# Optimization experiments

Hardware: AMD Instinct MI355X
Metric: run time of the kernel (lower is better)

Reference implementation:

```python
import math
import jax, jax.numpy as jnp
import numpy as np

B, T, C, H = 2, 2048, 1024, 16
HD = C // H  # head dim = 64


def setup_inputs() -> dict:
    key = jax.random.key(0)
    k1, k2, k3 = jax.random.split(key, 3)
    x = jax.random.normal(k1, (B, T, C), dtype=jnp.float32)
    w_attn = jax.random.normal(k2, (C, 3 * C), dtype=jnp.float32) * (1.0 / math.sqrt(C))
    b_attn = jnp.zeros((3 * C,), dtype=jnp.float32)
    w_proj = jax.random.normal(k3, (C, C), dtype=jnp.float32) * (1.0 / math.sqrt(C))
    b_proj = jnp.zeros((C,), dtype=jnp.float32)
    return {"x": x, "w_attn": w_attn, "b_attn": b_attn, "w_proj": w_proj, "b_proj": b_proj}


def reference(x, w_attn, b_attn, w_proj, b_proj):
    b, t, c = x.shape
    hd = c // H
    # fused QKV projection: [B,T,3C]
    qkv = x @ w_attn + b_attn
    q, k, v = jnp.split(qkv, 3, axis=2)
    # [B,T,C] -> [B,H,T,hd]
    q = q.reshape(b, t, H, hd).transpose(0, 2, 1, 3)
    k = k.reshape(b, t, H, hd).transpose(0, 2, 1, 3)
    v = v.reshape(b, t, H, hd).transpose(0, 2, 1, 3)
    # scaled scores: [B,H,T,T]
    att = jnp.einsum("bhqd,bhkd->bhqk", q, k) * (1.0 / math.sqrt(hd))
    # causal mask: keep lower triangle, -inf elsewhere
    causal = jnp.tril(jnp.ones((t, t), dtype=bool))
    att = jnp.where(causal[None, None, :, :], att, jnp.float32(-jnp.inf))
    att = jax.nn.softmax(att, axis=-1)
    # attention-weighted values: [B,H,T,hd] -> [B,T,C]
    y = jnp.einsum("bhqk,bhkd->bhqd", att, v)
    y = y.transpose(0, 2, 1, 3).reshape(b, t, c)
    # output projection (dropout prob 0 => identity)
    return y @ w_proj + b_proj
```

## Files before the change

### kernel.cpp

```cpp
#include <hip/hip_runtime.h>
#include <type_traits>


typedef __bf16 bf16x8 __attribute__((ext_vector_type(8)));
typedef __bf16 bf16x4 __attribute__((ext_vector_type(4)));
typedef short shortx4 __attribute__((ext_vector_type(4)));
typedef float f32x4 __attribute__((ext_vector_type(4)));

#define B_ 2
#define T_ 2048
#define C_ 1024
#define H_ 16
#define HD_ 64
#define ROWS_ (B_ * T_)
#define N3C_ (3 * C_)

__device__ inline void gll16(const void* g, void* l) {
    __builtin_amdgcn_global_load_lds(
        (const __attribute__((address_space(1))) void*)g,
        (__attribute__((address_space(3))) void*)l, 16, 0, 0);
}

__device__ inline f32x4 mfma16x16x16(bf16x4 a, bf16x4 b, f32x4 c) {
#if defined(__HIP_DEVICE_COMPILE__)
#if __has_builtin(__builtin_amdgcn_mfma_f32_16x16x16bf16_1k)
    return __builtin_amdgcn_mfma_f32_16x16x16bf16_1k(
        __builtin_bit_cast(shortx4, a), __builtin_bit_cast(shortx4, b), c, 0, 0, 0);
#else
    return __builtin_amdgcn_mfma_f32_16x16x16_bf16(
        __builtin_bit_cast(shortx4, a), __builtin_bit_cast(shortx4, b), c, 0, 0, 0);
#endif
#else
    (void)a; (void)b;
    return c;
#endif
}

__device__ inline float v_exp2(float x) {
#if defined(__HIP_DEVICE_COMPILE__)
    float r;
    asm("v_exp_f32 %0, %1" : "=v"(r) : "v"(x));
    return r;
#else
    return x;
#endif
}

__device__ inline float bias_at(const void* bias, int col, bool in_bf) {
    return in_bf ? (float)((const __bf16*)bias)[col] : ((const float*)bias)[col];
}

__global__ void detect_dtype(const unsigned* __restrict__ w, unsigned* __restrict__ flag) {
    int lane = threadIdx.x & 63;
    int cnt = 0;
#pragma unroll
    for (int i = 0; i < 4; ++i) {
        unsigned v = w[lane * 4 + i];
        unsigned e = (v >> 7) & 0xFFu;
        cnt += (e >= 116u && e <= 134u) ? 1 : 0;
    }
#pragma unroll
    for (int off = 1; off < 64; off <<= 1) cnt += __shfl_xor(cnt, off, 64);
    if (lane == 0) *flag = (cnt >= 128) ? 1u : 0u;
}

__global__ __launch_bounds__(256) void convert_to_bf16(const void* __restrict__ src,
                                                       __bf16* __restrict__ dst, int n,
                                                       const unsigned* __restrict__ flag) {
    bool isbf = (*flag != 0u);
    int i = (blockIdx.x * 256 + threadIdx.x) * 8;
    if (i >= n) return;
    if (isbf) {
        *(bf16x8*)&dst[i] = *(const bf16x8*)((const __bf16*)src + i);
    } else {
        const float4* s4 = (const float4*)src;
        float4 a = s4[i / 4], b = s4[i / 4 + 1];
        bf16x8 v;
        v[0] = (__bf16)a.x; v[1] = (__bf16)a.y; v[2] = (__bf16)a.z; v[3] = (__bf16)a.w;
        v[4] = (__bf16)b.x; v[5] = (__bf16)b.y; v[6] = (__bf16)b.z; v[7] = (__bf16)b.w;
        *(bf16x8*)&dst[i] = v;
    }
}

__global__ __launch_bounds__(256) void transpose2(const void* __restrict__ wa,
                                                  __bf16* __restrict__ wat,
                                                  const void* __restrict__ wp,
                                                  __bf16* __restrict__ wpt,
                                                  const unsigned* __restrict__ flag) {
    int z = blockIdx.z;
    if (z && blockIdx.x >= 16) return;
    const void* src = z ? wp : wa;
    __bf16* dst = z ? wpt : wat;
    int R = C_, Cc = z ? C_ : N3C_;

    __shared__ __align__(16) __bf16 tile[64][65];
    bool isbf = (*flag != 0u);
    const __bf16* sb = (const __bf16*)src;
    const float* sf = (const float*)src;
    int cb = blockIdx.x * 64, rb = blockIdx.y * 64;
    for (int i = threadIdx.x; i < 4096; i += 256) {
        int r = i >> 6, c = i & 63;
        size_t idx = (size_t)(rb + r) * Cc + cb + c;
        tile[r][c] = isbf ? sb[idx] : (__bf16)sf[idx];
    }
    __syncthreads();
    for (int i = threadIdx.x; i < 4096; i += 256) {
        int r = i >> 6, c = i & 63;
        dst[(size_t)(cb + r) * R + rb + c] = tile[c][r];
    }
}

__global__ __launch_bounds__(256) void gemm_qkv(const __bf16* __restrict__ A,
                                                const __bf16* __restrict__ Bt,
                                                const void* __restrict__ bias,
                                                __bf16* __restrict__ qg,
                                                __bf16* __restrict__ kg,
                                                __bf16* __restrict__ vn,
                                                const unsigned* __restrict__ flag) {
    const int K = C_;
    __shared__ __align__(16) __bf16 As[2 * 128 * 32];
    __shared__ __align__(16) __bf16 Bs[2 * 128 * 32];
    bool in_bf = (*flag != 0u);
    int tid = threadIdx.x;
    int wave = tid >> 6, lane = tid & 63;
    int quad = lane >> 4, l15 = lane & 15;
    int mb = blockIdx.y * 128, nb = blockIdx.x * 128;
    int wm = (wave >> 1) * 64, wn = (wave & 1) * 64;

    f32x4 acc[4][4] = {};

    for (int k0 = 0; k0 < K; k0 += 64) {
        __syncthreads();
#pragma unroll
        for (int q = 0; q < 4; ++q) {
            int kh = q >> 1;
            int idx = (q & 1) * 256 + tid;
            int r = idx >> 2, c32 = (idx & 3) * 8;
            gll16(&A[(size_t)(mb + r) * K + k0 + kh * 32 + c32], &As[(q * 256 + wave * 64) * 8]);
            gll16(&Bt[(size_t)(nb + r) * K + k0 + kh * 32 + c32], &Bs[(q * 256 + wave * 64) * 8]);
        }
        __syncthreads();

#pragma unroll
        for (int ks = 0; ks < 2; ++ks) {
            bf16x8 af[4], bfr[4];
#pragma unroll
            for (int i = 0; i < 4; ++i)
                af[i] = *(const bf16x8*)&As[ks * 4096 + (wm + i * 16 + l15) * 32 + quad * 8];
#pragma unroll
            for (int j = 0; j < 4; ++j)
                bfr[j] = *(const bf16x8*)&Bs[ks * 4096 + (wn + j * 16 + l15) * 32 + quad * 8];
#pragma unroll
            for (int i = 0; i < 4; ++i)
#pragma unroll
                for (int j = 0; j < 4; ++j)
                    acc[i][j] = __builtin_amdgcn_mfma_f32_16x16x32_bf16(af[i], bfr[j], acc[i][j], 0, 0, 0);
        }
    }

#pragma unroll
    for (int i = 0; i < 4; ++i) {
        int row = mb + wm + i * 16 + quad * 4;
#pragma unroll
        for (int j = 0; j < 4; ++j) {
            int col = nb + wn + j * 16 + l15;
            float bv = bias_at(bias, col, in_bf);
            int region = col >> 10;
            int cc = col & 1023;
            int hh = cc >> 6, hd = cc & 63;
            __bf16* dstbase = (region == 0) ? qg : (region == 1) ? kg : vn;
#pragma unroll
            for (int r = 0; r < 4; ++r) {
                int rr = row + r;
                int t = rr & (T_ - 1), bb = rr >> 11;
                float val = acc[i][j][r] + bv;
                size_t bh = (size_t)(bb * H_ + hh);
                dstbase[(bh * T_ + t) * HD_ + hd] = (__bf16)val;
            }
        }
    }
}

__global__ __launch_bounds__(256) void transpose_v(const __bf16* __restrict__ vn,
                                                   __bf16* __restrict__ vtg) {
    __shared__ __align__(16) __bf16 tile[64][65];
    int bh = blockIdx.y, t0 = blockIdx.x * 64;
    const __bf16* src = vn + ((size_t)bh * T_ + t0) * HD_;
    __bf16* dst = vtg + (size_t)bh * HD_ * T_ + t0;
    int tid = threadIdx.x;
    int r = tid >> 3, c = (tid & 7) * 8;
    *(bf16x8*)&tile[r][c] = *(const bf16x8*)&src[(size_t)r * HD_ + c];
    *(bf16x8*)&tile[r + 32][c] = *(const bf16x8*)&src[(size_t)(r + 32) * HD_ + c];
    __syncthreads();
#pragma unroll
    for (int it = 0; it < 2; ++it) {
        int idx = it * 256 + tid;
        int hd = idx >> 3, ch = (idx & 7) * 8;
        bf16x8 v;
#pragma unroll
        for (int e = 0; e < 8; ++e) v[e] = tile[ch + e][hd];
        *(bf16x8*)&dst[(size_t)hd * T_ + ch] = v;
    }
}

__global__ __launch_bounds__(256) void attn_kernel(const __bf16* __restrict__ qg,
                                                   const __bf16* __restrict__ kg,
                                                   const __bf16* __restrict__ vtg,
                                                   __bf16* __restrict__ y) {
    const int LDT = 72;
    __shared__ __align__(16) __bf16 Ks[64 * LDT];
    __shared__ __align__(16) __bf16 Vts[64 * LDT];

    int tid = threadIdx.x, wave = tid >> 6, lane = tid & 63;
    int quad = lane >> 4, l15 = lane & 15;
    int p = blockIdx.x;
    int qA = p, qB = 31 - p;
    int bh = blockIdx.y;
    int b = bh >> 4, h = bh & 15;

    const __bf16* qbh = qg + (size_t)bh * T_ * HD_;
    const __bf16* kbh = kg + (size_t)bh * T_ * HD_;
    const __bf16* vbh = vtg + (size_t)bh * HD_ * T_;

    int rowA = qA * 64 + wave * 16;
    int rowB = qB * 64 + wave * 16;

    bf16x8 qfA[2], qfB[2];
#pragma unroll
    for (int ks = 0; ks < 2; ++ks) {
        qfA[ks] = *(const bf16x8*)&qbh[(size_t)(rowA + l15) * HD_ + ks * 32 + quad * 8];
        qfB[ks] = *(const bf16x8*)&qbh[(size_t)(rowB + l15) * HD_ + ks * 32 + quad * 8];
    }

    f32x4 oA[4] = {}, oB[4] = {};
    f32x4 laccA = {}, laccB = {};
    const float C1 = 0.125f * 1.44269504088896340736f;
    const float C2 = 12.0f * 1.44269504088896340736f;

    bf16x4 onesb;
#pragma unroll
    for (int e = 0; e < 4; ++e) onesb[e] = (__bf16)1.0f;

    bf16x8 kf[4][2];
    bf16x4 vf[4][4];

    auto tile_step = [&](auto diagc, const bf16x8* qf, int rowX, int kbase,
                         f32x4* o, f32x4& lacc) {
        constexpr bool DIAG = decltype(diagc)::value;
        f32x4 s[4] = {};
#pragma unroll
        for (int ks = 0; ks < 2; ++ks)
#pragma unroll
            for (int j = 0; j < 4; ++j)
                s[j] = __builtin_amdgcn_mfma_f32_16x16x32_bf16(kf[j][ks], qf[ks], s[j], 0, 0, 0);

        int q = rowX + l15;
#pragma unroll
        for (int j = 0; j < 4; ++j) {
            bf16x4 pb;
#pragma unroll
            for (int r = 0; r < 4; ++r) {
                float e = v_exp2(fmaf(s[j][r], C1, -C2));
                if (DIAG) {
                    int key = kbase + j * 16 + quad * 4 + r;
                    e = (key > q) ? 0.f : e;
                }
                pb[r] = (__bf16)e;
            }
#pragma unroll
            for (int i = 0; i < 4; ++i)
                o[i] = mfma16x16x16(pb, vf[i][j], o[i]);
            lacc = mfma16x16x16(pb, onesb, lacc);
        }
    };

    for (int kt = 0; kt <= qB; ++kt) {
        int kbase = kt * 64;
        __syncthreads();
#pragma unroll
        for (int t = 0; t < 2; ++t) {
            int vid = tid + t * 256;
            int r = vid >> 3, c = (vid & 7) * 8;
            *(bf16x8*)&Ks[r * LDT + c]  = *(const bf16x8*)&kbh[(size_t)(kbase + r) * HD_ + c];
            *(bf16x8*)&Vts[r * LDT + c] = *(const bf16x8*)&vbh[(size_t)r * T_ + kbase + c];
        }
        __syncthreads();

#pragma unroll
        for (int j = 0; j < 4; ++j)
#pragma unroll
            for (int ks = 0; ks < 2; ++ks)
                kf[j][ks] = *(const bf16x8*)&Ks[(j * 16 + l15) * LDT + ks * 32 + quad * 8];
#pragma unroll
        for (int i = 0; i < 4; ++i)
#pragma unroll
            for (int j = 0; j < 4; ++j)
                vf[i][j] = *(const bf16x4*)&Vts[(i * 16 + l15) * LDT + j * 16 + quad * 4];

        if (kt == qB) tile_step(std::true_type{},  qfB, rowB, kbase, oB, laccB);
        else          tile_step(std::false_type{}, qfB, rowB, kbase, oB, laccB);
        if (kt < qA)       tile_step(std::false_type{}, qfA, rowA, kbase, oA, laccA);
        else if (kt == qA) tile_step(std::true_type{},  qfA, rowA, kbase, oA, laccA);
    }

#pragma unroll
    for (int i = 0; i < 4; ++i) {
        int col = h * HD_ + i * 16 + l15;
#pragma unroll
        for (int r = 0; r < 4; ++r) {
            y[(size_t)(b * T_ + rowA + quad * 4 + r) * C_ + col] = (__bf16)(oA[i][r] / laccA[r]);
            y[(size_t)(b * T_ + rowB + quad * 4 + r) * C_ + col] = (__bf16)(oB[i][r] / laccB[r]);
        }
    }
}

__global__ __launch_bounds__(256) void gemm_proj(const __bf16* __restrict__ A,
                                                 const __bf16* __restrict__ Bt,
                                                 const void* __restrict__ bias,
                                                 void* __restrict__ Cv,
                                                 const unsigned* __restrict__ flag) {
    const int K = C_, N = C_;
    __shared__ __align__(16) __bf16 As[2 * 64 * 32];
    __shared__ __align__(16) __bf16 Bs[2 * 128 * 32];
    bool in_bf = (*flag != 0u);
    int tid = threadIdx.x;
    int wave = tid >> 6, lane = tid & 63;
    int quad = lane >> 4, l15 = lane & 15;
    int mb = blockIdx.y * 64, nb = blockIdx.x * 128;
    int wm = (wave >> 1) * 32, wn = (wave & 1) * 64;

    f32x4 acc[2][4] = {};

    for (int k0 = 0; k0 < K; k0 += 64) {
        __syncthreads();
#pragma unroll
        for (int q = 0; q < 2; ++q) {
            int r = tid >> 2, c32 = (tid & 3) * 8;
            gll16(&A[(size_t)(mb + r) * K + k0 + q * 32 + c32], &As[(q * 256 + wave * 64) * 8]);
        }
#pragma unroll
        for (int q = 0; q < 4; ++q) {
            int kh = q >> 1;
            int idx = (q & 1) * 256 + tid;
            int r = idx >> 2, c32 = (idx & 3) * 8;
            gll16(&Bt[(size_t)(nb + r) * K + k0 + kh * 32 + c32], &Bs[(q * 256 + wave * 64) * 8]);
        }
        __syncthreads();

#pragma unroll
        for (int ks = 0; ks < 2; ++ks) {
            bf16x8 af[2], bfr[4];
#pragma unroll
            for (int i = 0; i < 2; ++i)
                af[i] = *(const bf16x8*)&As[ks * 2048 + (wm + i * 16 + l15) * 32 + quad * 8];
#pragma unroll
            for (int j = 0; j < 4; ++j)
                bfr[j] = *(const bf16x8*)&Bs[ks * 4096 + (wn + j * 16 + l15) * 32 + quad * 8];
#pragma unroll
            for (int i = 0; i < 2; ++i)
#pragma unroll
                for (int j = 0; j < 4; ++j)
                    acc[i][j] = __builtin_amdgcn_mfma_f32_16x16x32_bf16(af[i], bfr[j], acc[i][j], 0, 0, 0);
        }
    }

#pragma unroll
    for (int i = 0; i < 2; ++i) {
        int row = mb + wm + i * 16 + quad * 4;
#pragma unroll
        for (int j = 0; j < 4; ++j) {
            int col = nb + wn + j * 16 + l15;
            float bv = bias_at(bias, col, in_bf);
#pragma unroll
            for (int r = 0; r < 4; ++r) {
                float val = acc[i][j][r] + bv;
                size_t off = (size_t)(row + r) * N + col;
                if (in_bf) ((__bf16*)Cv)[off] = (__bf16)val;
                else       ((float*)Cv)[off]  = val;
            }
        }
    }
}

extern "C" void kernel_launch(void* const* d_in, const int* in_sizes, int n_in,
                              void* d_out, int out_size, void* d_ws, size_t ws_size,
                              hipStream_t stream) {
    const void* x      = d_in[0];
    const void* w_attn = d_in[1];
    const void* b_attn = d_in[2];
    const void* w_proj = d_in[3];
    const void* b_proj = d_in[4];

    char* base = (char*)d_ws;
    unsigned* flag = (unsigned*)base;
    __bf16* xc   = (__bf16*)(base + 256);
    __bf16* wat  = xc + (size_t)ROWS_ * C_;
    __bf16* wpt  = wat + (size_t)N3C_ * C_;
    __bf16* qg   = wpt + (size_t)C_ * C_;
    __bf16* kg   = qg + (size_t)B_ * H_ * T_ * HD_;
    __bf16* vn   = kg + (size_t)B_ * H_ * T_ * HD_;
    __bf16* vtg  = vn + (size_t)B_ * H_ * T_ * HD_;
    __bf16* yb   = vtg + (size_t)B_ * H_ * T_ * HD_;

    detect_dtype<<<1, 64, 0, stream>>>((const unsigned*)x, flag);

    convert_to_bf16<<<(ROWS_ * C_ / 8 + 255) / 256, 256, 0, stream>>>(x, xc, ROWS_ * C_, flag);

    transpose2<<<dim3(N3C_ / 64, C_ / 64, 2), 256, 0, stream>>>(w_attn, wat, w_proj, wpt, flag);

    gemm_qkv<<<dim3(N3C_ / 128, ROWS_ / 128), 256, 0, stream>>>(
        xc, wat, b_attn, qg, kg, vn, flag);

    transpose_v<<<dim3(T_ / 64, B_ * H_), 256, 0, stream>>>(vn, vtg);

    attn_kernel<<<dim3(16, B_ * H_), 256, 0, stream>>>(qg, kg, vtg, yb);

    gemm_proj<<<dim3(C_ / 128, ROWS_ / 64), 256, 0, stream>>>(yb, wpt, b_proj, d_out, flag);
}
```

Baseline: 195.1 us.

## Fuse prep kernels, inline dtype detection, split attention work across more blocks

Merges the dtype-detect, input-convert and weight-transpose launches into a single prep kernel, with every kernel re-detecting dtype from x instead of reading a flag. The attention grid doubles so that each wave owns one 16-row query strip: waves 0-1 take the light tile and waves 2-3 the heavy one. K/V tiles are prefetched into registers one step ahead, and launch bounds target 4 blocks per CU. This cuts launch count and raises attention occupancy. The cost is idle waves on the short-tile side during later iterations and duplicated detection reads.

```diff
diff --git a/kernel.cpp b/kernel.cpp
--- a/kernel.cpp
+++ b/kernel.cpp
@@ -46,11 +46,8 @@
 #endif
 }
 
-__device__ inline float bias_at(const void* bias, int col, bool in_bf) {
-    return in_bf ? (float)((const __bf16*)bias)[col] : ((const float*)bias)[col];
-}
-
-__global__ void detect_dtype(const unsigned* __restrict__ w, unsigned* __restrict__ flag) {
+__device__ inline bool self_detect(const void* x) {
+    const unsigned* w = (const unsigned*)x;
     int lane = threadIdx.x & 63;
     int cnt = 0;
 #pragma unroll
@@ -61,43 +58,49 @@
     }
 #pragma unroll
     for (int off = 1; off < 64; off <<= 1) cnt += __shfl_xor(cnt, off, 64);
-    if (lane == 0) *flag = (cnt >= 128) ? 1u : 0u;
-}
-
-__global__ __launch_bounds__(256) void convert_to_bf16(const void* __restrict__ src,
-                                                       __bf16* __restrict__ dst, int n,
-                                                       const unsigned* __restrict__ flag) {
-    bool isbf = (*flag != 0u);
-    int i = (blockIdx.x * 256 + threadIdx.x) * 8;
-    if (i >= n) return;
-    if (isbf) {
-        *(bf16x8*)&dst[i] = *(const bf16x8*)((const __bf16*)src + i);
+    return cnt >= 128;
+}
+
+__device__ inline float bias_at(const void* bias, int col, bool in_bf) {
+    return in_bf ? (float)((const __bf16*)bias)[col] : ((const float*)bias)[col];
+}
+
+__global__ __launch_bounds__(256) void prep(const void* __restrict__ x,
+                                            __bf16* __restrict__ xc,
+                                            const void* __restrict__ wa,
+                                            __bf16* __restrict__ wat,
+                                            const void* __restrict__ wp,
+                                            __bf16* __restrict__ wpt) {
+    __shared__ __align__(16) __bf16 tile[64][65];
+    bool isbf = self_detect(x);
+    int id = blockIdx.x;
+    if (id < 2048) {
+        int i = (id * 256 + threadIdx.x) * 8;
+        if (isbf) {
+            *(bf16x8*)&xc[i] = *(const bf16x8*)((const __bf16*)x + i);
+        } else {
+            const float4* s4 = (const float4*)x;
+            float4 a = s4[i / 4], b = s4[i / 4 + 1];
+            bf16x8 v;
+            v[0] = (__bf16)a.x; v[1] = (__bf16)a.y; v[2] = (__bf16)a.z; v[3] = (__bf16)a.w;
+            v[4] = (__bf16)b.x; v[5] = (__bf16)b.y; v[6] = (__bf16)b.z; v[7] = (__bf16)b.w;
+            *(bf16x8*)&xc[i] = v;
+        }
+        return;
+    }
+    const void* src; __bf16* dst; int Cc, bx, by;
+    if (id < 2048 + 768) {
+        int id2 = id - 2048;
+        src = wa; dst = wat; Cc = N3C_;
+        bx = id2 % 48; by = id2 / 48;
     } else {
-        const float4* s4 = (const float4*)src;
-        float4 a = s4[i / 4], b = s4[i / 4 + 1];
-        bf16x8 v;
-        v[0] = (__bf16)a.x; v[1] = (__bf16)a.y; v[2] = (__bf16)a.z; v[3] = (__bf16)a.w;
-        v[4] = (__bf16)b.x; v[5] = (__bf16)b.y; v[6] = (__bf16)b.z; v[7] = (__bf16)b.w;
-        *(bf16x8*)&dst[i] = v;
-    }
-}
-
-__global__ __launch_bounds__(256) void transpose2(const void* __restrict__ wa,
-                                                  __bf16* __restrict__ wat,
-                                                  const void* __restrict__ wp,
-                                                  __bf16* __restrict__ wpt,
-                                                  const unsigned* __restrict__ flag) {
-    int z = blockIdx.z;
-    if (z && blockIdx.x >= 16) return;
-    const void* src = z ? wp : wa;
-    __bf16* dst = z ? wpt : wat;
-    int R = C_, Cc = z ? C_ : N3C_;
-
-    __shared__ __align__(16) __bf16 tile[64][65];
-    bool isbf = (*flag != 0u);
+        int id3 = id - 2048 - 768;
+        src = wp; dst = wpt; Cc = C_;
+        bx = id3 % 16; by = id3 / 16;
+    }
     const __bf16* sb = (const __bf16*)src;
     const float* sf = (const float*)src;
-    int cb = blockIdx.x * 64, rb = blockIdx.y * 64;
+    int cb = bx * 64, rb = by * 64;
     for (int i = threadIdx.x; i < 4096; i += 256) {
         int r = i >> 6, c = i & 63;
         size_t idx = (size_t)(rb + r) * Cc + cb + c;
@@ -106,7 +109,7 @@
     __syncthreads();
     for (int i = threadIdx.x; i < 4096; i += 256) {
         int r = i >> 6, c = i & 63;
-        dst[(size_t)(cb + r) * R + rb + c] = tile[c][r];
+        dst[(size_t)(cb + r) * C_ + rb + c] = tile[c][r];
     }
 }
 
@@ -116,11 +119,11 @@
                                                 __bf16* __restrict__ qg,
                                                 __bf16* __restrict__ kg,
                                                 __bf16* __restrict__ vn,
-                                                const unsigned* __restrict__ flag) {
+                                                const void* __restrict__ xs) {
     const int K = C_;
     __shared__ __align__(16) __bf16 As[2 * 128 * 32];
     __shared__ __align__(16) __bf16 Bs[2 * 128 * 32];
-    bool in_bf = (*flag != 0u);
+    bool in_bf = self_detect(xs);
     int tid = threadIdx.x;
     int wave = tid >> 6, lane = tid & 63;
     int quad = lane >> 4, l15 = lane & 15;
@@ -203,37 +206,38 @@
     }
 }
 
-__global__ __launch_bounds__(256) void attn_kernel(const __bf16* __restrict__ qg,
-                                                   const __bf16* __restrict__ kg,
-                                                   const __bf16* __restrict__ vtg,
-                                                   __bf16* __restrict__ y) {
+__global__ __launch_bounds__(256, 4) void attn_kernel(const __bf16* __restrict__ qg,
+                                                      const __bf16* __restrict__ kg,
+                                                      const __bf16* __restrict__ vtg,
+                                                      __bf16* __restrict__ y) {
     const int LDT = 72;
     __shared__ __align__(16) __bf16 Ks[64 * LDT];
     __shared__ __align__(16) __bf16 Vts[64 * LDT];
 
     int tid = threadIdx.x, wave = tid >> 6, lane = tid & 63;
     int quad = lane >> 4, l15 = lane & 15;
-    int p = blockIdx.x;
+    int bx = blockIdx.x;
+    int bh = blockIdx.y;
+    int px = (bx + bh) & 31;
+    int p = px >> 1, half = px & 1;
     int qA = p, qB = 31 - p;
-    int bh = blockIdx.y;
     int b = bh >> 4, h = bh & 15;
+
+    bool isB = (wave >= 2);
+    int myq = isB ? qB : qA;
+    int myrow = myq * 64 + half * 32 + (wave & 1) * 16;
 
     const __bf16* qbh = qg + (size_t)bh * T_ * HD_;
     const __bf16* kbh = kg + (size_t)bh * T_ * HD_;
     const __bf16* vbh = vtg + (size_t)bh * HD_ * T_;
 
-    int rowA = qA * 64 + wave * 16;
-    int rowB = qB * 64 + wave * 16;
-
-    bf16x8 qfA[2], qfB[2];
-#pragma unroll
-    for (int ks = 0; ks < 2; ++ks) {
-        qfA[ks] = *(const bf16x8*)&qbh[(size_t)(rowA + l15) * HD_ + ks * 32 + quad * 8];
-        qfB[ks] = *(const bf16x8*)&qbh[(size_t)(rowB + l15) * HD_ + ks * 32 + quad * 8];
-    }
-
-    f32x4 oA[4] = {}, oB[4] = {};
-    f32x4 laccA = {}, laccB = {};
+    bf16x8 qf[2];
+#pragma unroll
+    for (int ks = 0; ks < 2; ++ks)
+        qf[ks] = *(const bf16x8*)&qbh[(size_t)(myrow + l15) * HD_ + ks * 32 + quad * 8];
+
+    f32x4 o[4] = {};
+    f32x4 lacc = {};
     const float C1 = 0.125f * 1.44269504088896340736f;
     const float C2 = 12.0f * 1.44269504088896340736f;
 
@@ -241,76 +245,77 @@
 #pragma unroll
     for (int e = 0; e < 4; ++e) onesb[e] = (__bf16)1.0f;
 
-    bf16x8 kf[4][2];
-    bf16x4 vf[4][4];
-
-    auto tile_step = [&](auto diagc, const bf16x8* qf, int rowX, int kbase,
-                         f32x4* o, f32x4& lacc) {
-        constexpr bool DIAG = decltype(diagc)::value;
-        f32x4 s[4] = {};
-#pragma unroll
-        for (int ks = 0; ks < 2; ++ks)
+    int sr0 = tid >> 3, sc0 = (tid & 7) * 8;
+    int sr1 = (tid + 256) >> 3, sc1 = ((tid + 256) & 7) * 8;
+
+    bf16x8 pk[2], pv[2];
+    auto prefetch = [&](int kbase) {
+        pk[0] = *(const bf16x8*)&kbh[(size_t)(kbase + sr0) * HD_ + sc0];
+        pk[1] = *(const bf16x8*)&kbh[(size_t)(kbase + sr1) * HD_ + sc1];
+        pv[0] = *(const bf16x8*)&vbh[(size_t)sr0 * T_ + kbase + sc0];
+        pv[1] = *(const bf16x8*)&vbh[(size_t)sr1 * T_ + kbase + sc1];
+    };
+    prefetch(0);
+
+    for (int kt = 0; kt <= qB; ++kt) {
+        __syncthreads();
+        *(bf16x8*)&Ks[sr0 * LDT + sc0]  = pk[0];
+        *(bf16x8*)&Ks[sr1 * LDT + sc1]  = pk[1];
+        *(bf16x8*)&Vts[sr0 * LDT + sc0] = pv[0];
+        *(bf16x8*)&Vts[sr1 * LDT + sc1] = pv[1];
+        __syncthreads();
+        if (kt < qB) prefetch((kt + 1) * 64);
+
+        if (kt <= myq) {
+            int kbase = kt * 64;
+            bf16x8 kf[4][2];
 #pragma unroll
             for (int j = 0; j < 4; ++j)
-                s[j] = __builtin_amdgcn_mfma_f32_16x16x32_bf16(kf[j][ks], qf[ks], s[j], 0, 0, 0);
-
-        int q = rowX + l15;
-#pragma unroll
-        for (int j = 0; j < 4; ++j) {
-            bf16x4 pb;
-#pragma unroll
-            for (int r = 0; r < 4; ++r) {
-                float e = v_exp2(fmaf(s[j][r], C1, -C2));
-                if (DIAG) {
-                    int key = kbase + j * 16 + quad * 4 + r;
-                    e = (key > q) ? 0.f : e;
+#pragma unroll
+                for (int ks = 0; ks < 2; ++ks)
+                    kf[j][ks] = *(const bf16x8*)&Ks[(j * 16 + l15) * LDT + ks * 32 + quad * 8];
+            bf16x4 vf[4][4];
+#pragma unroll
+            for (int i = 0; i < 4; ++i)
+#pragma unroll
+                for (int j = 0; j < 4; ++j)
+                    vf[i][j] = *(const bf16x4*)&Vts[(i * 16 + l15) * LDT + j * 16 + quad * 4];
+
+            f32x4 s[4] = {};
+#pragma unroll
+            for (int ks = 0; ks < 2; ++ks)
+#pragma unroll
+                for (int j = 0; j < 4; ++j)
+                    s[j] = __builtin_amdgcn_mfma_f32_16x16x32_bf16(kf[j][ks], qf[ks], s[j], 0, 0, 0);
+
+            bool diag = (kt == myq);
+            int q = myrow + l15;
+#pragma unroll
+            for (int j = 0; j < 4; ++j) {
+                bf16x4 pb;
+#pragma unroll
+                for (int r = 0; r < 4; ++r) {
+                    float e = v_exp2(fmaf(s[j][r], C1, -C2));
+                    if (diag) {
+                        int key = kbase + j * 16 + quad * 4 + r;
+                        e = (key > q) ? 0.f : e;
+                    }
+                    pb[r] = (__bf16)e;
                 }
-                pb[r] = (__bf16)e;
+#pragma unroll
+                for (int i = 0; i < 4; ++i)
+                    o[i] = mfma16x16x16(pb, vf[i][j], o[i]);
+                lacc = mfma16x16x16(pb, onesb, lacc);
             }
-#pragma unroll
-            for (int i = 0; i < 4; ++i)
-                o[i] = mfma16x16x16(pb, vf[i][j], o[i]);
-            lacc = mfma16x16x16(pb, onesb, lacc);
-        }
-    };
-
-    for (int kt = 0; kt <= qB; ++kt) {
-        int kbase = kt * 64;
-        __syncthreads();
-#pragma unroll
-        for (int t = 0; t < 2; ++t) {
-            int vid = tid + t * 256;
-            int r = vid >> 3, c = (vid & 7) * 8;
-            *(bf16x8*)&Ks[r * LDT + c]  = *(const bf16x8*)&kbh[(size_t)(kbase + r) * HD_ + c];
-            *(bf16x8*)&Vts[r * LDT + c] = *(const bf16x8*)&vbh[(size_t)r * T_ + kbase + c];
-        }
-        __syncthreads();
-
-#pragma unroll
-        for (int j = 0; j < 4; ++j)
-#pragma unroll
-            for (int ks = 0; ks < 2; ++ks)
-                kf[j][ks] = *(const bf16x8*)&Ks[(j * 16 + l15) * LDT + ks * 32 + quad * 8];
-#pragma unroll
-        for (int i = 0; i < 4; ++i)
-#pragma unroll
-            for (int j = 0; j < 4; ++j)
-                vf[i][j] = *(const bf16x4*)&Vts[(i * 16 + l15) * LDT + j * 16 + quad * 4];
-
-        if (kt == qB) tile_step(std::true_type{},  qfB, rowB, kbase, oB, laccB);
-        else          tile_step(std::false_type{}, qfB, rowB, kbase, oB, laccB);
-        if (kt < qA)       tile_step(std::false_type{}, qfA, rowA, kbase, oA, laccA);
-        else if (kt == qA) tile_step(std::true_type{},  qfA, rowA, kbase, oA, laccA);
+        }
     }
 
 #pragma unroll
     for (int i = 0; i < 4; ++i) {
         int col = h * HD_ + i * 16 + l15;
 #pragma unroll
-        for (int r = 0; r < 4; ++r) {
-            y[(size_t)(b * T_ + rowA + quad * 4 + r) * C_ + col] = (__bf16)(oA[i][r] / laccA[r]);
-            y[(size_t)(b * T_ + rowB + quad * 4 + r) * C_ + col] = (__bf16)(oB[i][r] / laccB[r]);
-        }
+        for (int r = 0; r < 4; ++r)
+            y[(size_t)(b * T_ + myrow + quad * 4 + r) * C_ + col] = (__bf16)(o[i][r] / lacc[r]);
     }
 }
 
@@ -318,11 +323,11 @@
                                                  const __bf16* __restrict__ Bt,
                                                  const void* __restrict__ bias,
                                                  void* __restrict__ Cv,
-                                                 const unsigned* __restrict__ flag) {
+                                                 const void* __restrict__ xs) {
     const int K = C_, N = C_;
     __shared__ __align__(16) __bf16 As[2 * 64 * 32];
     __shared__ __align__(16) __bf16 Bs[2 * 128 * 32];
-    bool in_bf = (*flag != 0u);
+    bool in_bf = self_detect(xs);
     int tid = threadIdx.x;
     int wave = tid >> 6, lane = tid & 63;
     int quad = lane >> 4, l15 = lane & 15;
@@ -392,7 +397,6 @@
     const void* b_proj = d_in[4];
 
     char* base = (char*)d_ws;
-    unsigned* flag = (unsigned*)base;
     __bf16* xc   = (__bf16*)(base + 256);
     __bf16* wat  = xc + (size_t)ROWS_ * C_;
     __bf16* wpt  = wat + (size_t)N3C_ * C_;
@@ -402,18 +406,14 @@
     __bf16* vtg  = vn + (size_t)B_ * H_ * T_ * HD_;
     __bf16* yb   = vtg + (size_t)B_ * H_ * T_ * HD_;
 
-    detect_dtype<<<1, 64, 0, stream>>>((const unsigned*)x, flag);
-
-    convert_to_bf16<<<(ROWS_ * C_ / 8 + 255) / 256, 256, 0, stream>>>(x, xc, ROWS_ * C_, flag);
-
-    transpose2<<<dim3(N3C_ / 64, C_ / 64, 2), 256, 0, stream>>>(w_attn, wat, w_proj, wpt, flag);
+    prep<<<2048 + 768 + 256, 256, 0, stream>>>(x, xc, w_attn, wat, w_proj, wpt);
 
     gemm_qkv<<<dim3(N3C_ / 128, ROWS_ / 128), 256, 0, stream>>>(
-        xc, wat, b_attn, qg, kg, vn, flag);
+        xc, wat, b_attn, qg, kg, vn, x);
 
     transpose_v<<<dim3(T_ / 64, B_ * H_), 256, 0, stream>>>(vn, vtg);
 
-    attn_kernel<<<dim3(16, B_ * H_), 256, 0, stream>>>(qg, kg, vtg, yb);
-
-    gemm_proj<<<dim3(C_ / 128, ROWS_ / 64), 256, 0, stream>>>(yb, wpt, b_proj, d_out, flag);
-}
+    attn_kernel<<<dim3(32, B_ * H_), 256, 0, stream>>>(qg, kg, vtg, yb);
+
+    gemm_proj<<<dim3(C_ / 128, ROWS_ / 64), 256, 0, stream>>>(yb, wpt, b_proj, d_out, x);
+}
```

Result: no change. 196.4 us (+0.6%).
